# Optimization experiments

Measured on AMD Instinct MI355X. Metric: run time of the kernel, lower is better.

## Reference

```python
import jax, jax.numpy as jnp
import numpy as np

B, C, T = 8, 1024, 2048
CI = C // 2
BN_EPS = 1e-5


def setup_inputs() -> dict:
    key = jax.random.key(0)
    ks = jax.random.split(key, 12)
    sc_in = 1.0 / np.sqrt(C)
    sc_ci = 1.0 / np.sqrt(CI)
    return {
        "x": jax.random.normal(ks[0], (B, C, T), dtype=jnp.float32),
        "Wq_w": jax.random.normal(ks[1], (CI, C), dtype=jnp.float32) * sc_in,
        "Wq_b": jax.random.normal(ks[2], (CI,), dtype=jnp.float32) * 0.02,
        "Wk_w": jax.random.normal(ks[3], (CI, C), dtype=jnp.float32) * sc_in,
        "Wk_b": jax.random.normal(ks[4], (CI,), dtype=jnp.float32) * 0.02,
        "Wv_w": jax.random.normal(ks[5], (CI, C), dtype=jnp.float32) * sc_in,
        "Wv_b": jax.random.normal(ks[6], (CI,), dtype=jnp.float32) * 0.02,
        "Wo_w": jax.random.normal(ks[7], (C, CI), dtype=jnp.float32) * sc_ci,
        "Wo_b": jax.random.normal(ks[8], (C,), dtype=jnp.float32) * 0.02,
        "gamma": jax.random.normal(ks[9], (C,), dtype=jnp.float32) * 0.1 + 1.0,
        "beta": jax.random.normal(ks[10], (C,), dtype=jnp.float32) * 0.02,
    }


def reference(x, Wq_w, Wq_b, Wk_w, Wk_b, Wv_w, Wv_b, Wo_w, Wo_b, gamma, beta):
    # 1x1 Conv1d projections == channel-wise linear maps
    q = jnp.einsum('oc,bct->bto', Wq_w, x) + Wq_b          # [B, T, Ci]
    k = jnp.einsum('oc,bct->bot', Wk_w, x) + Wk_b[:, None]  # [B, Ci, T]
    v = jnp.einsum('oc,bct->bto', Wv_w, x) + Wv_b          # [B, T, Ci]

    s = jnp.einsum('bqc,bck->bqk', q, k)                   # [B, Tq, Tk], unscaled
    sim = jax.nn.softmax(s, axis=-2)                        # softmax over QUERY axis
    y = jnp.einsum('bqk,bkc->bcq', sim, v)                  # [B, Ci, T]

    wy = jnp.einsum('oc,bct->bot', Wo_w, y) + Wo_b[:, None]  # [B, C, T]

    # BatchNorm1d in training mode: stats over (batch, time) per channel
    mean = jnp.mean(wy, axis=(0, 2), keepdims=True)
    var = jnp.var(wy, axis=(0, 2), keepdims=True)
    wy_bn = (wy - mean) * jax.lax.rsqrt(var + BN_EPS)
    wy_bn = wy_bn * gamma[None, :, None] + beta[None, :, None]

    return wy_bn + x
```

## Files before the change

### kernel.cpp

```cpp
#include <hip/hip_runtime.h>
#include <hip/hip_fp16.h>

typedef _Float16 f16;
typedef f16 f16x8 __attribute__((ext_vector_type(8)));
typedef f16 f16x4 __attribute__((ext_vector_type(4)));
typedef float f32x4 __attribute__((ext_vector_type(4)));

constexpr int Bb = 8, Cc = 1024, Tt = 2048, Ci = 512;
constexpr float BN_EPS = 1e-5f;

__device__ __forceinline__ void gload16(const f16* g, f16* l) {
  __builtin_amdgcn_global_load_lds(
      (const __attribute__((address_space(1))) void*)g,
      (__attribute__((address_space(3))) void*)l, 16, 0, 0);
}

__global__ __launch_bounds__(256)
void cvt_kernel(const float* __restrict__ src, f16* __restrict__ dst, int n4) {
  int i = blockIdx.x * blockDim.x + threadIdx.x;
  if (i < n4) {
    float4 v = *((const float4*)src + i);
    f16x4 h;
    h[0] = (f16)v.x; h[1] = (f16)v.y; h[2] = (f16)v.z; h[3] = (f16)v.w;
    *((f16x4*)dst + i) = h;
  }
}

__global__ __launch_bounds__(256)
void cvtT_kernel(const float* __restrict__ x, f16* __restrict__ xT) {
  __shared__ float tile[64][68];
  const int b = blockIdx.z, c0 = blockIdx.y * 64, t0 = blockIdx.x * 64;
  const int tid = threadIdx.x;
  const float* xp = x + ((long)b * Cc + c0) * Tt + t0;
  {
    int r = tid >> 4, c4 = (tid & 15) * 4;
    #pragma unroll
    for (int it = 0; it < 4; it++) {
      float4 v = *(const float4*)(xp + (long)(r + it * 16) * Tt + c4);
      *(float4*)&tile[r + it * 16][c4] = v;
    }
  }
  __syncthreads();
  f16* op = xT + ((long)b * Tt + t0) * Cc + c0;
  {
    int c8 = (tid & 7) * 8;
    #pragma unroll
    for (int it = 0; it < 2; it++) {
      int t = (tid >> 3) + it * 32;
      f16x8 o;
      #pragma unroll
      for (int jj = 0; jj < 8; jj++) o[jj] = (f16)tile[c8 + jj][t];
      *(f16x8*)(op + (long)t * Cc + c8) = o;
    }
  }
}

template<int BIAS_MODE, bool DO_MAX>
__global__ __launch_bounds__(512, 2)
void gemm8p(const f16* __restrict__ A, const f16* __restrict__ B,
            f16* __restrict__ C, const float* __restrict__ bias,
            unsigned* __restrict__ gmax,
            int K, int lda, int ldb, int ldc, long sA, long sB, long sC,
            int nx, int ny)
{
  extern __shared__ f16 lds[];
  constexpr int TILE_A = 256 * 64;
  constexpr int TILE_B = 128 * 64;
  constexpr int TILE   = TILE_A + TILE_B;

  const int per = gridDim.x >> 3;
  const int nid = (blockIdx.x & 7) * per + (blockIdx.x >> 3);
  const int bz = nid / (nx * ny);
  const int rem = nid - bz * nx * ny;
  const int by = rem / nx, bx = rem - by * nx;

  const int tid = threadIdx.x, lane = tid & 63, wv = tid >> 6;
  const int bm0 = by * 256, bn0 = bx * 128;
  const int wm = (wv >> 1) * 64, wn = (wv & 1) * 64;
  const f16* Ab = A + (long)bz * sA + (long)bm0 * lda;
  const f16* Bt = B + (long)bz * sB + (long)bn0 * ldb;
  C += (long)bz * sC;

  const int r16 = lane & 15, khi = lane >> 4;
  const int sw = (r16 & 7) << 4;

  auto stA = [&](int slot, int k0, int r) {
    int L = (r * 512 + tid) * 16;
    int G = L ^ (((L >> 7) & 7) << 4);
    gload16(Ab + (long)(G >> 7) * lda + k0 + ((G & 127) >> 1),
            lds + (long)slot * TILE + (r * 512 + wv * 64) * 8);
  };
  auto stB = [&](int slot, int k0, int r) {
    int L = (r * 512 + tid) * 16;
    int G = L ^ (((L >> 7) & 7) << 4);
    gload16(Bt + (long)(G >> 7) * ldb + k0 + ((G & 127) >> 1),
            lds + (long)slot * TILE + TILE_A + (r * 512 + wv * 64) * 8);
  };

  f32x4 acc[4][4] = {};
  const int nt = K >> 6;

  #pragma unroll
  for (int r = 0; r < 4; r++) stA(0, 0, r);
  #pragma unroll
  for (int r = 0; r < 2; r++) stB(0, 0, r);
  #pragma unroll
  for (int r = 0; r < 4; r++) stA(1, 64, r);
  #pragma unroll
  for (int r = 0; r < 2; r++) stB(1, 64, r);
  asm volatile("s_waitcnt vmcnt(6)" ::: "memory");
  __builtin_amdgcn_s_barrier();

  for (int t = 0; t < nt; t++) {
    const int slot = t % 3;
    const int nslot = (t + 2) % 3;
    const int k2 = (t + 2) << 6;
    const bool st = (t + 2) < nt;
    const char* baseA = (const char*)(lds + (long)slot * TILE);
    const char* baseB = (const char*)(lds + (long)slot * TILE + TILE_A);

    if (st) {
      stA(nslot, k2, 0); stA(nslot, k2, 1); stA(nslot, k2, 2); stA(nslot, k2, 3);
      stB(nslot, k2, 0); stB(nslot, k2, 1);
    }

    f16x8 af0[4], bf0[4], af1[4], bf1[4];
    #pragma unroll
    for (int i = 0; i < 4; i++) {
      af0[i] = *(const f16x8*)(baseA + (((wm + i * 16 + r16) * 128 + khi * 16) ^ sw));
      af1[i] = *(const f16x8*)(baseA + (((wm + i * 16 + r16) * 128 + 64 + khi * 16) ^ sw));
    }
    #pragma unroll
    for (int j = 0; j < 4; j++) {
      bf0[j] = *(const f16x8*)(baseB + (((wn + j * 16 + r16) * 128 + khi * 16) ^ sw));
      bf1[j] = *(const f16x8*)(baseB + (((wn + j * 16 + r16) * 128 + 64 + khi * 16) ^ sw));
    }

    __builtin_amdgcn_s_setprio(1);
    #pragma unroll
    for (int i = 0; i < 4; i++)
      #pragma unroll
      for (int j = 0; j < 4; j++) {
        acc[i][j] = __builtin_amdgcn_mfma_f32_16x16x32_f16(af0[i], bf0[j], acc[i][j], 0, 0, 0);
        acc[i][j] = __builtin_amdgcn_mfma_f32_16x16x32_f16(af1[i], bf1[j], acc[i][j], 0, 0, 0);
      }
    __builtin_amdgcn_s_setprio(0);

    __builtin_amdgcn_sched_barrier(0);
    if (st) asm volatile("s_waitcnt vmcnt(6)" ::: "memory");
    else    asm volatile("s_waitcnt vmcnt(0)" ::: "memory");
    __builtin_amdgcn_s_barrier();
  }

  const int rg = khi * 4;
  float cmx[4] = {-3e38f, -3e38f, -3e38f, -3e38f};
  #pragma unroll
  for (int i = 0; i < 4; i++) {
    const int row0 = bm0 + wm + i * 16 + rg;
    #pragma unroll
    for (int r = 0; r < 4; r++) {
      const int row = row0 + r;
      const float br = (BIAS_MODE == 1) ? bias[row] : 0.0f;
      #pragma unroll
      for (int j = 0; j < 4; j++) {
        const int col = bn0 + wn + j * 16 + r16;
        float v = acc[i][j][r] + ((BIAS_MODE == 2) ? bias[col] : br);
        C[(long)row * ldc + col] = (f16)v;
        if (DO_MAX) cmx[j] = fmaxf(cmx[j], v);
      }
    }
  }
  if (DO_MAX) {
    #pragma unroll
    for (int j = 0; j < 4; j++) {
      float mx = cmx[j];
      mx = fmaxf(mx, __shfl_xor(mx, 16));
      mx = fmaxf(mx, __shfl_xor(mx, 32));
      if (khi == 0) {
        const int col = bn0 + wn + j * 16 + r16;
        unsigned u = __float_as_uint(mx);
        unsigned key = (u & 0x80000000u) ? ~u : (u | 0x80000000u);
        atomicMax(gmax + (long)bz * ldc + col, key);
      }
    }
  }
}

__global__ __launch_bounds__(256)
void colsum_kernel(f16* __restrict__ E, const unsigned* __restrict__ gmax,
                   float* __restrict__ sums) {
  const int b = blockIdx.z;
  const int kt = blockIdx.x * 256 + threadIdx.x;
  const long q0 = (long)blockIdx.y * 128;
  unsigned key = gmax[b * Tt + kt];
  float m = (key & 0x80000000u) ? __uint_as_float(key ^ 0x80000000u)
                                : __uint_as_float(~key);
  f16* p = E + ((long)b * Tt + q0) * Tt + kt;
  float s = 0.f;
  #pragma unroll 4
  for (int q = 0; q < 128; q++) {
    float e = __expf((float)p[(long)q * Tt] - m);
    p[(long)q * Tt] = (f16)e;
    s += e;
  }
  atomicAdd(sums + b * Tt + kt, s);
}

__global__ __launch_bounds__(256)
void vscale_kernel(f16* __restrict__ Vt, const float* __restrict__ sums) {
  long i = ((long)blockIdx.x * 256 + threadIdx.x) * 8;
  int kt = (int)(i & (Tt - 1));
  int b = (int)(i >> 20);
  f16x8 v = *(f16x8*)(Vt + i);
  const float* sp = sums + b * Tt + kt;
  #pragma unroll
  for (int j = 0; j < 8; j++)
    v[j] = (f16)((float)v[j] * __fdividef(1.0f, sp[j]));
  *(f16x8*)(Vt + i) = v;
}

__global__ __launch_bounds__(256)
void bnstat_kernel(const f16* __restrict__ wy, float* __restrict__ bsum,
                   float* __restrict__ bsq) {
  const int c = blockIdx.x, tid = threadIdx.x;
  float s1 = 0.f, s2 = 0.f;
  for (int b = 0; b < Bb; b++) {
    f16x8 v = *((const f16x8*)(wy + ((long)b * Cc + c) * Tt) + tid);
    #pragma unroll
    for (int jj = 0; jj < 8; jj++) { float f = (float)v[jj]; s1 += f; s2 += f * f; }
  }
  #pragma unroll
  for (int off = 1; off < 64; off <<= 1) {
    s1 += __shfl_xor(s1, off);
    s2 += __shfl_xor(s2, off);
  }
  __shared__ float l1[4], l2[4];
  const int w = tid >> 6;
  if ((tid & 63) == 0) { l1[w] = s1; l2[w] = s2; }
  __syncthreads();
  if (tid == 0) {
    bsum[c] = (l1[0] + l1[1]) + (l1[2] + l1[3]);
    bsq[c]  = (l2[0] + l2[1]) + (l2[2] + l2[3]);
  }
}

__global__ __launch_bounds__(256)
void final_kernel(const f16* __restrict__ wy, const float* __restrict__ x,
                  const float* __restrict__ gamma, const float* __restrict__ beta,
                  const float* __restrict__ bsum, const float* __restrict__ bsq,
                  float* __restrict__ out)
{
  long i = ((long)blockIdx.x * blockDim.x + threadIdx.x) * 4;
  int c = (int)((i >> 11) & (Cc - 1));
  const float cnt = (float)Bb * (float)Tt;
  float mean = bsum[c] / cnt;
  float var  = bsq[c] / cnt - mean * mean;
  float sc = rsqrtf(var + BN_EPS) * gamma[c];
  float sh = beta[c] - mean * sc;
  f16x4 w = *(const f16x4*)(wy + i);
  float4 xv = *(const float4*)(x + i);
  float4 o;
  o.x = (float)w[0] * sc + sh + xv.x;
  o.y = (float)w[1] * sc + sh + xv.y;
  o.z = (float)w[2] * sc + sh + xv.z;
  o.w = (float)w[3] * sc + sh + xv.w;
  *(float4*)(out + i) = o;
}

extern "C" void kernel_launch(void* const* d_in, const int* in_sizes, int n_in,
                              void* d_out, int out_size, void* d_ws, size_t ws_size,
                              hipStream_t stream) {
  const float* x    = (const float*)d_in[0];
  const float* Wq_w = (const float*)d_in[1];
  const float* Wq_b = (const float*)d_in[2];
  const float* Wk_w = (const float*)d_in[3];
  const float* Wk_b = (const float*)d_in[4];
  const float* Wv_w = (const float*)d_in[5];
  const float* Wv_b = (const float*)d_in[6];
  const float* Wo_w = (const float*)d_in[7];
  const float* Wo_b = (const float*)d_in[8];
  const float* gamma = (const float*)d_in[9];
  const float* beta  = (const float*)d_in[10];
  float* out = (float*)d_out;

  constexpr long SZ_XT = (long)Bb * Tt * Cc;
  constexpr long SZ_Q  = (long)Bb * Tt * Ci;
  constexpr long SZ_S  = (long)Bb * Tt * Tt;
  constexpr long SZ_W  = (long)Ci * Cc;

  f16* ws = (f16*)d_ws;
  f16* xT  = ws;
  f16* QK  = xT + SZ_XT;
  f16* Vt  = QK + SZ_XT;
  f16* Sq  = Vt + SZ_Q;
  f16* Y   = Sq + SZ_S;
  f16* wy  = Y + SZ_Q;
  f16* wqk = wy + SZ_XT;
  f16* wv  = wqk + 2 * SZ_W;
  f16* wo  = wv + SZ_W;
  unsigned* gmax = (unsigned*)(wo + SZ_W);
  float* sums = (float*)(gmax + (long)Bb * Tt);
  float* bsum = sums + (long)Bb * Tt;
  float* bsq  = bsum + Cc;
  float* qkb  = bsq + Cc;

  constexpr int LDSB = (256 * 64 + 128 * 64) * 3 * 2;
  hipFuncSetAttribute(reinterpret_cast<const void*>(gemm8p<2, false>),
                      hipFuncAttributeMaxDynamicSharedMemorySize, LDSB);
  hipFuncSetAttribute(reinterpret_cast<const void*>(gemm8p<1, false>),
                      hipFuncAttributeMaxDynamicSharedMemorySize, LDSB);
  hipFuncSetAttribute(reinterpret_cast<const void*>(gemm8p<0, true>),
                      hipFuncAttributeMaxDynamicSharedMemorySize, LDSB);
  hipFuncSetAttribute(reinterpret_cast<const void*>(gemm8p<0, false>),
                      hipFuncAttributeMaxDynamicSharedMemorySize, LDSB);

  hipMemsetAsync(gmax, 0, (long)Bb * Tt * 2 * sizeof(float), stream);
  hipMemcpyAsync(qkb, Wq_b, Ci * sizeof(float), hipMemcpyDeviceToDevice, stream);
  hipMemcpyAsync(qkb + Ci, Wk_b, Ci * sizeof(float), hipMemcpyDeviceToDevice, stream);

  cvt_kernel<<<(int)(SZ_W / 4 / 256), 256, 0, stream>>>(Wq_w, wqk, (int)(SZ_W / 4));
  cvt_kernel<<<(int)(SZ_W / 4 / 256), 256, 0, stream>>>(Wk_w, wqk + SZ_W, (int)(SZ_W / 4));
  cvt_kernel<<<(int)(SZ_W / 4 / 256), 256, 0, stream>>>(Wv_w, wv, (int)(SZ_W / 4));
  cvt_kernel<<<(int)(SZ_W / 4 / 256), 256, 0, stream>>>(Wo_w, wo, (int)(SZ_W / 4));
  cvtT_kernel<<<dim3(Tt / 64, Cc / 64, Bb), 256, 0, stream>>>(x, xT);

  gemm8p<2, false><<<8 * 8 * Bb, 512, LDSB, stream>>>(
      xT, wqk, QK, qkb, nullptr,
      Cc, Cc, Cc, 1024, (long)Tt * Cc, 0, (long)Tt * 1024, 8, 8);

  gemm8p<1, false><<<16 * 2 * Bb, 512, LDSB, stream>>>(
      wv, xT, Vt, Wv_b, nullptr,
      Cc, Cc, Cc, Tt, 0, (long)Tt * Cc, (long)Ci * Tt, 16, 2);

  gemm8p<0, true><<<16 * 8 * Bb, 512, LDSB, stream>>>(
      QK, QK + 512, Sq, nullptr, gmax,
      Ci, 1024, 1024, Tt, (long)Tt * 1024, (long)Tt * 1024, (long)Tt * Tt, 16, 8);

  colsum_kernel<<<dim3(Tt / 256, Tt / 128, Bb), 256, 0, stream>>>(Sq, gmax, sums);

  vscale_kernel<<<(int)(SZ_Q / 8 / 256), 256, 0, stream>>>(Vt, sums);

  gemm8p<0, false><<<4 * 8 * Bb, 512, LDSB, stream>>>(
      Sq, Vt, Y, nullptr, nullptr,
      Tt, Tt, Tt, Ci, (long)Tt * Tt, (long)Ci * Tt, (long)Tt * Ci, 4, 8);

  gemm8p<1, false><<<16 * 4 * Bb, 512, LDSB, stream>>>(
      wo, Y, wy, Wo_b, nullptr,
      Ci, Ci, Ci, Tt, 0, (long)Tt * Ci, (long)Cc * Tt, 16, 4);

  bnstat_kernel<<<Cc, 256, 0, stream>>>(wy, bsum, bsq);
  final_kernel<<<(int)(SZ_XT / 4 / 256), 256, 0, stream>>>(
      wy, x, gamma, beta, bsum, bsq, out);
}
```

Measured before the change: 290.1 us.

## Add 256x256-tile double-buffered GEMM kernel for QK, scores, and output projection

Adds a new gemm256 kernel that uses 256x256 output tiles with 8 waves (2x4), each wave computing 128x64 using 16x16x32 MFMAs. It stages K=64 slabs into double-buffered LDS through direct global-to-LDS loads, splitting each slab into two halves so loads overlap compute. The QK projection, the score GEMM with column max, and the Wo projection switch to it with half as many blocks. The larger tiles are meant to raise arithmetic intensity and cut global traffic, at the cost of fewer blocks (wave-quantization risk) and more registers per thread.

```diff
diff --git a/kernel.cpp b/kernel.cpp
--- a/kernel.cpp
+++ b/kernel.cpp
@@ -51,6 +51,132 @@
       #pragma unroll
       for (int jj = 0; jj < 8; jj++) o[jj] = (f16)tile[c8 + jj][t];
       *(f16x8*)(op + (long)t * Cc + c8) = o;
+    }
+  }
+}
+
+template<int BIAS_MODE, bool DO_MAX>
+__global__ __launch_bounds__(512, 2)
+void gemm256(const f16* __restrict__ A, const f16* __restrict__ B,
+             f16* __restrict__ C, const float* __restrict__ bias,
+             unsigned* __restrict__ gmax,
+             int K, int lda, int ldb, int ldc, long sA, long sB, long sC,
+             int nx, int ny)
+{
+  extern __shared__ f16 lds[];
+  const int per = gridDim.x >> 3;
+  const int nid = (blockIdx.x & 7) * per + (blockIdx.x >> 3);
+  const int bz = nid / (nx * ny);
+  const int rem = nid - bz * nx * ny;
+  const int by = rem / nx, bx = rem - by * nx;
+
+  const int tid = threadIdx.x, lane = tid & 63, wv = tid >> 6;
+  const int bm0 = by * 256, bn0 = bx * 256;
+  const int wm = wv >> 2, wn = wv & 3;
+  const f16* Ab = A + (long)bz * sA + (long)bm0 * lda;
+  const f16* Bt = B + (long)bz * sB + (long)bn0 * ldb;
+  C += (long)bz * sC;
+  const int r16 = lane & 15, khi4 = lane >> 4;
+  const int trow = tid & 255, tkq = tid >> 8;
+
+  auto stA = [&](int sel, int q, int k0) {
+    gload16(Ab + (long)trow * lda + k0 + (2 * q + tkq) * 8,
+            lds + sel * 32768 + (q * 512 + wv * 64) * 8);
+  };
+  auto stB = [&](int sel, int q, int k0) {
+    gload16(Bt + (long)trow * ldb + k0 + (2 * q + tkq) * 8,
+            lds + sel * 32768 + 16384 + (q * 512 + wv * 64) * 8);
+  };
+
+  f32x4 acc[8][4] = {};
+  const int nt = K >> 6;
+  const int aoff = (khi4 * 256 + wm * 128 + r16) * 8;
+  const int boff = (khi4 * 256 + wn * 64 + r16) * 8;
+
+  stA(0, 0, 0); stA(0, 1, 0); stB(0, 0, 0); stB(0, 1, 0);
+  stA(0, 2, 0); stA(0, 3, 0); stB(0, 2, 0); stB(0, 3, 0);
+  stA(1, 0, 64); stA(1, 1, 64); stB(1, 0, 64); stB(1, 1, 64);
+  asm volatile("s_waitcnt vmcnt(8)" ::: "memory");
+  __builtin_amdgcn_s_barrier();
+
+  for (int t = 0; t < nt; t++) {
+    const int bsel = t & 1, nsel = bsel ^ 1;
+    const f16* lA = lds + bsel * 32768;
+    const f16* lB = lA + 16384;
+    f16x8 a[8], b[4];
+
+    if (t + 1 < nt) {
+      const int kn = (t + 1) << 6;
+      stA(nsel, 2, kn); stA(nsel, 3, kn); stB(nsel, 2, kn); stB(nsel, 3, kn);
+    }
+    #pragma unroll
+    for (int mi = 0; mi < 8; mi++) a[mi] = *(const f16x8*)(lA + aoff + mi * 128);
+    #pragma unroll
+    for (int nj = 0; nj < 4; nj++) b[nj] = *(const f16x8*)(lB + boff + nj * 128);
+    __builtin_amdgcn_s_setprio(1);
+    #pragma unroll
+    for (int mi = 0; mi < 8; mi++)
+      #pragma unroll
+      for (int nj = 0; nj < 4; nj++)
+        acc[mi][nj] = __builtin_amdgcn_mfma_f32_16x16x32_f16(a[mi], b[nj], acc[mi][nj], 0, 0, 0);
+    __builtin_amdgcn_s_setprio(0);
+    __builtin_amdgcn_sched_barrier(0);
+    if (t + 1 < nt) asm volatile("s_waitcnt vmcnt(8)" ::: "memory");
+    else            asm volatile("s_waitcnt vmcnt(0)" ::: "memory");
+    __builtin_amdgcn_s_barrier();
+
+    if (t + 2 < nt) {
+      const int kn = (t + 2) << 6;
+      stA(bsel, 0, kn); stA(bsel, 1, kn); stB(bsel, 0, kn); stB(bsel, 1, kn);
+    }
+    #pragma unroll
+    for (int mi = 0; mi < 8; mi++) a[mi] = *(const f16x8*)(lA + aoff + 8192 + mi * 128);
+    #pragma unroll
+    for (int nj = 0; nj < 4; nj++) b[nj] = *(const f16x8*)(lB + boff + 8192 + nj * 128);
+    __builtin_amdgcn_s_setprio(1);
+    #pragma unroll
+    for (int mi = 0; mi < 8; mi++)
+      #pragma unroll
+      for (int nj = 0; nj < 4; nj++)
+        acc[mi][nj] = __builtin_amdgcn_mfma_f32_16x16x32_f16(a[mi], b[nj], acc[mi][nj], 0, 0, 0);
+    __builtin_amdgcn_s_setprio(0);
+    __builtin_amdgcn_sched_barrier(0);
+    if (t + 2 < nt)      asm volatile("s_waitcnt vmcnt(8)" ::: "memory");
+    else if (t + 1 < nt) asm volatile("s_waitcnt vmcnt(4)" ::: "memory");
+    else                 asm volatile("s_waitcnt vmcnt(0)" ::: "memory");
+    __builtin_amdgcn_s_barrier();
+  }
+
+  const int rg = khi4 * 4;
+  float cmx[4] = {-3e38f, -3e38f, -3e38f, -3e38f};
+  #pragma unroll
+  for (int mi = 0; mi < 8; mi++) {
+    const int row0 = bm0 + wm * 128 + mi * 16 + rg;
+    #pragma unroll
+    for (int r = 0; r < 4; r++) {
+      const int row = row0 + r;
+      const float br = (BIAS_MODE == 1) ? bias[row] : 0.0f;
+      #pragma unroll
+      for (int nj = 0; nj < 4; nj++) {
+        const int col = bn0 + wn * 64 + nj * 16 + r16;
+        float v = acc[mi][nj][r] + ((BIAS_MODE == 2) ? bias[col] : br);
+        C[(long)row * ldc + col] = (f16)v;
+        if (DO_MAX) cmx[nj] = fmaxf(cmx[nj], v);
+      }
+    }
+  }
+  if (DO_MAX) {
+    #pragma unroll
+    for (int nj = 0; nj < 4; nj++) {
+      float mx = cmx[nj];
+      mx = fmaxf(mx, __shfl_xor(mx, 16));
+      mx = fmaxf(mx, __shfl_xor(mx, 32));
+      if (khi4 == 0) {
+        const int col = bn0 + wn * 64 + nj * 16 + r16;
+        unsigned u = __float_as_uint(mx);
+        unsigned key = (u & 0x80000000u) ? ~u : (u | 0x80000000u);
+        atomicMax(gmax + (long)bz * ldc + col, key);
+      }
     }
   }
 }
@@ -304,12 +430,15 @@
   float* bsq  = bsum + Cc;
   float* qkb  = bsq + Cc;
 
-  constexpr int LDSB = (256 * 64 + 128 * 64) * 3 * 2;
-  hipFuncSetAttribute(reinterpret_cast<const void*>(gemm8p<2, false>),
-                      hipFuncAttributeMaxDynamicSharedMemorySize, LDSB);
+  constexpr int LDSB  = (256 * 64 + 128 * 64) * 3 * 2;
+  constexpr int LDSB2 = 2 * 32768 * 2;
+  hipFuncSetAttribute(reinterpret_cast<const void*>(gemm256<2, false>),
+                      hipFuncAttributeMaxDynamicSharedMemorySize, LDSB2);
+  hipFuncSetAttribute(reinterpret_cast<const void*>(gemm256<1, false>),
+                      hipFuncAttributeMaxDynamicSharedMemorySize, LDSB2);
+  hipFuncSetAttribute(reinterpret_cast<const void*>(gemm256<0, true>),
+                      hipFuncAttributeMaxDynamicSharedMemorySize, LDSB2);
   hipFuncSetAttribute(reinterpret_cast<const void*>(gemm8p<1, false>),
-                      hipFuncAttributeMaxDynamicSharedMemorySize, LDSB);
-  hipFuncSetAttribute(reinterpret_cast<const void*>(gemm8p<0, true>),
                       hipFuncAttributeMaxDynamicSharedMemorySize, LDSB);
   hipFuncSetAttribute(reinterpret_cast<const void*>(gemm8p<0, false>),
                       hipFuncAttributeMaxDynamicSharedMemorySize, LDSB);
@@ -324,17 +453,17 @@
   cvt_kernel<<<(int)(SZ_W / 4 / 256), 256, 0, stream>>>(Wo_w, wo, (int)(SZ_W / 4));
   cvtT_kernel<<<dim3(Tt / 64, Cc / 64, Bb), 256, 0, stream>>>(x, xT);
 
-  gemm8p<2, false><<<8 * 8 * Bb, 512, LDSB, stream>>>(
+  gemm256<2, false><<<4 * 8 * Bb, 512, LDSB2, stream>>>(
       xT, wqk, QK, qkb, nullptr,
-      Cc, Cc, Cc, 1024, (long)Tt * Cc, 0, (long)Tt * 1024, 8, 8);
+      Cc, Cc, Cc, 1024, (long)Tt * Cc, 0, (long)Tt * 1024, 4, 8);
 
   gemm8p<1, false><<<16 * 2 * Bb, 512, LDSB, stream>>>(
       wv, xT, Vt, Wv_b, nullptr,
       Cc, Cc, Cc, Tt, 0, (long)Tt * Cc, (long)Ci * Tt, 16, 2);
 
-  gemm8p<0, true><<<16 * 8 * Bb, 512, LDSB, stream>>>(
+  gemm256<0, true><<<8 * 8 * Bb, 512, LDSB2, stream>>>(
       QK, QK + 512, Sq, nullptr, gmax,
-      Ci, 1024, 1024, Tt, (long)Tt * 1024, (long)Tt * 1024, (long)Tt * Tt, 16, 8);
+      Ci, 1024, 1024, Tt, (long)Tt * 1024, (long)Tt * 1024, (long)Tt * Tt, 8, 8);
 
   colsum_kernel<<<dim3(Tt / 256, Tt / 128, Bb), 256, 0, stream>>>(Sq, gmax, sums);
 
@@ -344,9 +473,9 @@
       Sq, Vt, Y, nullptr, nullptr,
       Tt, Tt, Tt, Ci, (long)Tt * Tt, (long)Ci * Tt, (long)Tt * Ci, 4, 8);
 
-  gemm8p<1, false><<<16 * 4 * Bb, 512, LDSB, stream>>>(
+  gemm256<1, false><<<8 * 4 * Bb, 512, LDSB2, stream>>>(
       wo, Y, wy, Wo_b, nullptr,
-      Ci, Ci, Ci, Tt, 0, (long)Tt * Ci, (long)Cc * Tt, 16, 4);
+      Ci, Ci, Ci, Tt, 0, (long)Tt * Ci, (long)Cc * Tt, 8, 4);
 
   bnstat_kernel<<<Cc, 256, 0, stream>>>(wy, bsum, bsq);
   final_kernel<<<(int)(SZ_XT / 4 / 256), 256, 0, stream>>>(
```

After: 311.1 us. 1.07x slower.
